# Performance work log

Measured on AMD Instinct MI355X. Metric: run time of the kernel, lower is better.

## Reference

```python
import jax, jax.numpy as jnp
import numpy as np

B, N, C, T, K = 32, 4096, 768, 1000, 20

def setup_inputs() -> dict:
    key = jax.random.key(0)
    k1, k2, k3, k4 = jax.random.split(key, 4)
    g_feat = jax.random.normal(k1, (B, 1, C), dtype=jnp.float32)
    inp = jax.random.normal(k2, (B, N, C), dtype=jnp.float32)
    tau = jax.random.uniform(k3, (1,), dtype=jnp.float32)
    text_embeddings = jax.random.normal(k4, (T, C), dtype=jnp.float32) * 0.01
    return {"g_feat": g_feat, "input": inp, "tau": tau, "text_embeddings": text_embeddings}


def reference(g_feat, input, tau, text_embeddings):
    feat = input  # [B, N, C]
    # 1x1 conv of global feature against text embeddings -> class logits [B, T]
    vg_logit = jnp.einsum('bc,tc->bt', g_feat[:, 0, :], text_embeddings)
    # top-20 candidate categories per image
    _, indices = jax.lax.top_k(vg_logit, K)              # [B, K]
    agg_text_features = text_embeddings[indices]          # [B, K, C] gather
    # per-pixel logits against the 20 gathered text embeddings
    seg_logit = jnp.exp(tau[0]) * jnp.einsum('bkc,bnc->bkn', agg_text_features, feat)  # [B, K, N]
    # hard (straight-through) softmax over candidate axis (dim=-2)
    y_soft = jax.nn.softmax(seg_logit, axis=-2)
    idx = jnp.argmax(seg_logit, axis=-2)                  # [B, N]
    y_hard = jnp.moveaxis(jax.nn.one_hot(idx, K, dtype=seg_logit.dtype), -1, -2)  # [B, K, N]
    attn = y_hard - jax.lax.stop_gradient(y_soft) + y_soft
    # normalize over pixel axis (assign_eps = 1.0)
    assign_attn = attn / (jnp.sum(attn, axis=-1, keepdims=True) + 1.0)
    # combine: [B, N, K] @ [B, K, C] -> [B, N, C]
    text_grids = jnp.einsum('bkn,bkc->bnc', assign_attn, agg_text_features)
    return text_grids
```

## Files before the change

kernel.cpp:

```cpp
#include <hip/hip_runtime.h>
#include <cfloat>

#define B_ 32
#define N_ 4096
#define C_ 768
#define T_ 1000
#define K_ 20

#define PXB 256
#define PHC 32
#define NPH (C_/PHC)
#define GAP_TH 1e-4f
#define MAXF 16384

typedef float f32x4 __attribute__((ext_vector_type(4)));
typedef int   i32x2 __attribute__((ext_vector_type(2)));
typedef short s16x8 __attribute__((ext_vector_type(8)));

__device__ __forceinline__ unsigned short bf_rne(float x) {
    unsigned u = __float_as_uint(x);
    return (unsigned short)((u + 0x7fffu + ((u >> 16) & 1u)) >> 16);
}

__global__ __launch_bounds__(256) void k1_logits(const float* __restrict__ g_feat,
                                                 const float* __restrict__ text,
                                                 double* __restrict__ logits,
                                                 int* __restrict__ cnt,
                                                 int* __restrict__ flagcnt) {
    int b = blockIdx.x;
    int wid = threadIdx.x >> 6, lane = threadIdx.x & 63;
    int t = blockIdx.y * 4 + wid;
    if (b == 0 && blockIdx.y == 0) {
        for (int i = threadIdx.x; i < B_ * K_; i += 256) cnt[i] = 0;
        if (threadIdx.x == 0) flagcnt[0] = 0;
    }
    const float* g = g_feat + b * C_;
    const float* e = text + t * C_;
    double s = 0.0;
    #pragma unroll
    for (int j = 0; j < 12; ++j) {
        int c = lane + 64 * j;
        s += (double)g[c] * (double)e[c];
    }
    #pragma unroll
    for (int m = 32; m; m >>= 1) s += __shfl_xor(s, m);
    if (lane == 0) logits[b * T_ + t] = s;
}

__global__ __launch_bounds__(256) void k1b_topk(const double* __restrict__ logits,
                                                const float* __restrict__ text,
                                                float* __restrict__ agg,
                                                unsigned short* __restrict__ Epk) {
    __shared__ unsigned short hiL[32 * C_];
    __shared__ unsigned short loL[32 * C_];
    __shared__ int ssel[K_];
    int b = blockIdx.x, tid = threadIdx.x, lane = tid & 63;
    if (tid < 64) {
        double v[16];
        #pragma unroll
        for (int j = 0; j < 16; ++j) {
            int t = lane + 64 * j;
            v[j] = (t < T_) ? logits[b * T_ + t] : -DBL_MAX;
        }
        for (int it = 0; it < K_; ++it) {
            double bv = -DBL_MAX; int bi = 0x7fffffff;
            #pragma unroll
            for (int j = 0; j < 16; ++j) {
                int t = lane + 64 * j;
                if (v[j] > bv) { bv = v[j]; bi = t; }
            }
            #pragma unroll
            for (int m = 32; m; m >>= 1) {
                double ov = __shfl_xor(bv, m); int oi = __shfl_xor(bi, m);
                if (ov > bv || (ov == bv && oi < bi)) { bv = ov; bi = oi; }
            }
            if (lane == 0) ssel[it] = bi;
            #pragma unroll
            for (int j = 0; j < 16; ++j) {
                int t = lane + 64 * j;
                if (t == bi) v[j] = -DBL_MAX;
            }
        }
    }
    __syncthreads();
    for (int i = tid; i < 32 * C_; i += 256) {
        int r = i / C_, c = i - r * C_;
        float v = (r < K_) ? text[ssel[r] * C_ + c] : 0.f;
        if (r < K_) agg[b * K_ * C_ + i] = v;
        unsigned u = __float_as_uint(v);
        float fh = __uint_as_float(u & 0xffff0000u);
        hiL[i] = (unsigned short)(u >> 16);
        loL[i] = bf_rne(v - fh);
    }
    __syncthreads();
    for (int i = tid; i < 24 * 256; i += 256) {
        int p = i >> 8, r = i & 255, f = r >> 6, ln = r & 63;
        int row = (f & 1) * 16 + (ln & 15);
        int col = p * 32 + (ln >> 4) * 8;
        const unsigned short* src = ((f < 2) ? hiL : loL) + row * C_ + col;
        *(s16x8*)(Epk + ((size_t)b * 6144 + i) * 8) = *(const s16x8*)src;
    }
}

__global__ __launch_bounds__(256, 4) void k2_argmax(const float* __restrict__ feat,
                                                    const unsigned short* __restrict__ Epk,
                                                    int* __restrict__ kidx,
                                                    int* __restrict__ cnt,
                                                    int* __restrict__ flagcnt,
                                                    int* __restrict__ flaglist) {
    __shared__ unsigned short hiT[PXB * PHC];
    __shared__ unsigned short loT[PXB * PHC];
    __shared__ int scnt[K_];
    int bx = blockIdx.x;
    int b = bx >> 4, tile = bx & 15;
    int n0 = tile * PXB;
    int tid = threadIdx.x, wid = tid >> 6, lane = tid & 63;
    if (tid < K_) scnt[tid] = 0;
    __syncthreads();

    const float* fb = feat + ((size_t)b * N_ + n0) * C_;
    const unsigned short* Eb = Epk + (size_t)b * 6144 * 8;
    int l3 = lane >> 3;
    int ch = lane & 7;
    int arow = lane & 15, acg = lane >> 4;

    f32x4 fr[8];
    auto LOADF = [&](int p) {
        #pragma unroll
        for (int i = 0; i < 8; ++i) {
            int row = wid * 64 + i * 8 + l3;
            fr[i] = *(const f32x4*)(fb + (size_t)row * C_ + p * PHC + ch * 4);
        }
    };
    auto CVTW = [&]() {
        int g = ch >> 1, h = ch & 1;
        #pragma unroll
        for (int i = 0; i < 8; ++i) {
            int row = wid * 64 + i * 8 + l3;
            unsigned u0 = __float_as_uint(fr[i].x), u1 = __float_as_uint(fr[i].y);
            unsigned u2 = __float_as_uint(fr[i].z), u3 = __float_as_uint(fr[i].w);
            unsigned ha = (u0 >> 16) | (u1 & 0xffff0000u);
            unsigned hb = (u2 >> 16) | (u3 & 0xffff0000u);
            unsigned la = (unsigned)bf_rne(fr[i].x - __uint_as_float(u0 & 0xffff0000u)) |
                          ((unsigned)bf_rne(fr[i].y - __uint_as_float(u1 & 0xffff0000u)) << 16);
            unsigned lb = (unsigned)bf_rne(fr[i].z - __uint_as_float(u2 & 0xffff0000u)) |
                          ((unsigned)bf_rne(fr[i].w - __uint_as_float(u3 & 0xffff0000u)) << 16);
            int a16 = row * PHC + ((g ^ (row & 3)) * 8) + h * 4;
            i32x2 hv = { (int)ha, (int)hb };
            i32x2 lv = { (int)la, (int)lb };
            *(i32x2*)&hiT[a16] = hv;
            *(i32x2*)&loT[a16] = lv;
        }
    };

    s16x8 Ach0, Ach1, Acl0, Acl1;
    auto LOADA = [&](int p) {
        const s16x8* ap = (const s16x8*)(Eb + (size_t)p * 256 * 8);
        Ach0 = ap[0 * 64 + lane];
        Ach1 = ap[1 * 64 + lane];
        Acl0 = ap[2 * 64 + lane];
        Acl1 = ap[3 * 64 + lane];
    };

    f32x4 acc0[4], acc1[4];
    #pragma unroll
    for (int i = 0; i < 4; ++i) { acc0[i] = (f32x4)0.f; acc1[i] = (f32x4)0.f; }

    LOADF(0);

    #pragma unroll 1
    for (int p = 0; p < NPH; ++p) {
        LOADA(p);
        asm volatile("s_waitcnt lgkmcnt(0)" ::: "memory");
        __builtin_amdgcn_sched_barrier(0);
        CVTW();
        if (p + 1 < NPH) LOADF(p + 1);
        asm volatile("s_waitcnt lgkmcnt(0)" ::: "memory");
        __builtin_amdgcn_sched_barrier(0);

        #pragma unroll
        for (int i = 0; i < 4; ++i) {
            int px = wid * 64 + i * 16 + arow;
            int a16 = px * PHC + (acg ^ (px & 3)) * 8;
            s16x8 Bh = *(const s16x8*)&hiT[a16];
            s16x8 Bl = *(const s16x8*)&loT[a16];
            acc0[i] = __builtin_amdgcn_mfma_f32_16x16x32_bf16(Ach0, Bh, acc0[i], 0, 0, 0);
            acc1[i] = __builtin_amdgcn_mfma_f32_16x16x32_bf16(Ach1, Bh, acc1[i], 0, 0, 0);
            acc0[i] = __builtin_amdgcn_mfma_f32_16x16x32_bf16(Ach0, Bl, acc0[i], 0, 0, 0);
            acc1[i] = __builtin_amdgcn_mfma_f32_16x16x32_bf16(Ach1, Bl, acc1[i], 0, 0, 0);
            acc0[i] = __builtin_amdgcn_mfma_f32_16x16x32_bf16(Acl0, Bh, acc0[i], 0, 0, 0);
            acc1[i] = __builtin_amdgcn_mfma_f32_16x16x32_bf16(Acl1, Bh, acc1[i], 0, 0, 0);
        }
    }

    #pragma unroll
    for (int i = 0; i < 4; ++i) {
        int kb = acg * 4;
        float m1 = acc0[i][0]; int i1 = kb; float m2 = -FLT_MAX;
        #pragma unroll
        for (int r = 1; r < 4; ++r) {
            float v = acc0[i][r];
            if (v > m1) { m2 = m1; m1 = v; i1 = kb + r; }
            else if (v > m2) m2 = v;
        }
        if (acg == 0) {
            #pragma unroll
            for (int r = 0; r < 4; ++r) {
                float v = acc1[i][r];
                if (v > m1) { m2 = m1; m1 = v; i1 = 16 + r; }
                else if (v > m2) m2 = v;
            }
        }
        #pragma unroll
        for (int s = 16; s < 64; s <<= 1) {
            float om1 = __shfl_xor(m1, s); int oi1 = __shfl_xor(i1, s);
            float om2 = __shfl_xor(m2, s);
            if (om1 > m1 || (om1 == m1 && oi1 < i1)) { m2 = fmaxf(m1, om2); m1 = om1; i1 = oi1; }
            else { m2 = fmaxf(m2, om1); }
        }
        if (lane < 16) {
            int n = n0 + wid * 64 + i * 16 + lane;
            kidx[b * N_ + n] = i1;
            atomicAdd(&scnt[i1], 1);
            if (m1 - m2 < GAP_TH) {
                int pos = atomicAdd(flagcnt, 1);
                if (pos < MAXF) flaglist[pos] = b * N_ + n;
            }
        }
    }
    __syncthreads();
    if (tid < K_) atomicAdd(&cnt[b * K_ + tid], scnt[tid]);
}

__global__ __launch_bounds__(256) void k25_refine(const float* __restrict__ feat,
                                                  const float* __restrict__ agg,
                                                  int* __restrict__ kidx,
                                                  int* __restrict__ cnt,
                                                  const int* __restrict__ flagcnt,
                                                  const int* __restrict__ flaglist) {
    int wid = threadIdx.x >> 6, lane = threadIdx.x & 63;
    int wg = blockIdx.x * 4 + wid;
    int nf = flagcnt[0]; if (nf > MAXF) nf = MAXF;
    for (int e = wg; e < nf; e += gridDim.x * 4) {
        int pix = flaglist[e];
        int b = pix >> 12;
        const float* fr = feat + (size_t)pix * C_;
        const float* ebase = agg + b * K_ * C_;
        double fd[12];
        #pragma unroll
        for (int j = 0; j < 12; ++j) fd[j] = (double)fr[lane + 64 * j];
        double best = -DBL_MAX; int bi = 0;
        for (int k = 0; k < K_; ++k) {
            const float* er = ebase + k * C_;
            double s = 0.0;
            #pragma unroll
            for (int j = 0; j < 12; ++j) s += fd[j] * (double)er[lane + 64 * j];
            #pragma unroll
            for (int m = 32; m; m >>= 1) s += __shfl_xor(s, m);
            if (s > best) { best = s; bi = k; }
        }
        if (lane == 0) {
            int old = kidx[pix];
            if (old != bi) {
                kidx[pix] = bi;
                atomicSub(&cnt[b * K_ + old], 1);
                atomicAdd(&cnt[b * K_ + bi], 1);
            }
        }
    }
}

__global__ __launch_bounds__(256) void k3s_scale(const float* __restrict__ agg,
                                                 const int* __restrict__ cnt,
                                                 float* __restrict__ sagg) {
    __shared__ float sc[K_];
    int b = blockIdx.x, tid = threadIdx.x;
    if (tid < K_) sc[tid] = 1.0f / ((float)cnt[b * K_ + tid] + 1.0f);
    __syncthreads();
    const f32x4* a4 = (const f32x4*)(agg + (size_t)b * K_ * C_);
    f32x4* s4 = (f32x4*)(sagg + (size_t)b * K_ * C_);
    #pragma unroll 1
    for (int i = tid; i < K_ * (C_ / 4); i += 256) {
        int k = i / (C_ / 4);
        s4[i] = a4[i] * sc[k];
    }
}

__global__ __launch_bounds__(256) void k4_out(const float* __restrict__ sagg,
                                              const int* __restrict__ kidx,
                                              float* __restrict__ out) {
    int wid = threadIdx.x >> 6, lane = threadIdx.x & 63;
    int wg = blockIdx.x * 4 + wid;
    int base = wg * 8;
    int b = base >> 12;
    int kk[8];
    #pragma unroll
    for (int i = 0; i < 8; ++i) kk[i] = kidx[base + i];
    const f32x4* sagg4 = (const f32x4*)sagg;
    f32x4* out4 = (f32x4*)out;

    f32x4 va0, va1, va2, vb0, vb1, vb2;
    {
        const f32x4* a4 = sagg4 + (size_t)(b * K_ + kk[0]) * (C_ / 4);
        va0 = a4[lane]; va1 = a4[lane + 64]; va2 = a4[lane + 128];
    }
    #pragma unroll
    for (int i = 0; i < 8; ++i) {
        if (i + 1 < 8) {
            const f32x4* a4 = sagg4 + (size_t)(b * K_ + kk[i + 1]) * (C_ / 4);
            vb0 = a4[lane]; vb1 = a4[lane + 64]; vb2 = a4[lane + 128];
        }
        f32x4* o4 = out4 + (size_t)(base + i) * (C_ / 4);
        o4[lane] = va0; o4[lane + 64] = va1; o4[lane + 128] = va2;
        va0 = vb0; va1 = vb1; va2 = vb2;
    }
}

extern "C" void kernel_launch(void* const* d_in, const int* in_sizes, int n_in,
                              void* d_out, int out_size, void* d_ws, size_t ws_size,
                              hipStream_t stream) {
    const float* g_feat = (const float*)d_in[0];
    const float* feat   = (const float*)d_in[1];
    const float* text   = (const float*)d_in[3];
    float* out = (float*)d_out;

    char* ws = (char*)d_ws;
    double* logits        = (double*)(ws + 0);
    float*  agg           = (float*) (ws + 262144);
    int*    cnt           = (int*)   (ws + 2230784);
    int*    flagc         = (int*)   (ws + 2233344);
    int*    flagl         = (int*)   (ws + 2233408);
    int*    kidx          = (int*)   (ws + 2301504);
    unsigned short* Epk   = (unsigned short*)(ws + 2825792);
    float*  sagg          = (float*) (ws + 5971520);

    k1_logits<<<dim3(32, 250), 256, 0, stream>>>(g_feat, text, logits, cnt, flagc);
    k1b_topk<<<32, 256, 0, stream>>>(logits, text, agg, Epk);
    k2_argmax<<<32 * 16, 256, 0, stream>>>(feat, Epk, kidx, cnt, flagc, flagl);
    k25_refine<<<1024, 256, 0, stream>>>(feat, agg, kidx, cnt, flagc, flagl);
    k3s_scale<<<32, 256, 0, stream>>>(agg, cnt, sagg);
    k4_out<<<4096, 256, 0, stream>>>(sagg, kidx, out);
}
```

Before: 272.3 us.

## Load feature tiles directly into MFMA B-fragments, dropping LDS staging in argmax kernel

The argmax kernel now has each wavefront own 16 pixels and load feature values straight from global memory in the MFMA B-operand layout, converting them to hi/lo bf16 in registers. This removes the LDS transpose buffers, the LDS writes and reads, and the waitcnt barriers. The grid grows to 2048 blocks and the occupancy hint rises to 6. The trade-off is that each lane's global loads are now only 32 bytes per row across 16 rows, which coalesces less well. The per-wave A-fragment reloads from Epk also happen four times as often relative to the pixels processed.

```diff
diff --git a/kernel.cpp b/kernel.cpp
--- a/kernel.cpp
+++ b/kernel.cpp
@@ -7,14 +7,13 @@
 #define T_ 1000
 #define K_ 20
 
-#define PXB 256
 #define PHC 32
 #define NPH (C_/PHC)
 #define GAP_TH 1e-4f
 #define MAXF 16384
 
 typedef float f32x4 __attribute__((ext_vector_type(4)));
-typedef int   i32x2 __attribute__((ext_vector_type(2)));
+typedef int   i32x4 __attribute__((ext_vector_type(4)));
 typedef short s16x8 __attribute__((ext_vector_type(8)));
 
 __device__ __forceinline__ unsigned short bf_rne(float x) {
@@ -102,130 +101,101 @@
     }
 }
 
-__global__ __launch_bounds__(256, 4) void k2_argmax(const float* __restrict__ feat,
+__global__ __launch_bounds__(256, 6) void k2_argmax(const float* __restrict__ feat,
                                                     const unsigned short* __restrict__ Epk,
                                                     int* __restrict__ kidx,
                                                     int* __restrict__ cnt,
                                                     int* __restrict__ flagcnt,
                                                     int* __restrict__ flaglist) {
-    __shared__ unsigned short hiT[PXB * PHC];
-    __shared__ unsigned short loT[PXB * PHC];
     __shared__ int scnt[K_];
-    int bx = blockIdx.x;
-    int b = bx >> 4, tile = bx & 15;
-    int n0 = tile * PXB;
     int tid = threadIdx.x, wid = tid >> 6, lane = tid & 63;
     if (tid < K_) scnt[tid] = 0;
     __syncthreads();
 
-    const float* fb = feat + ((size_t)b * N_ + n0) * C_;
+    int gw = blockIdx.x * 4 + wid;
+    int b  = gw >> 8;
+    int n0 = (gw & 255) * 16;
+    int prow = lane & 15;
+    int g    = lane >> 4;
+    const float* fp0 = feat + ((size_t)b * N_ + n0 + prow) * C_ + g * 8;
     const unsigned short* Eb = Epk + (size_t)b * 6144 * 8;
-    int l3 = lane >> 3;
-    int ch = lane & 7;
-    int arow = lane & 15, acg = lane >> 4;
-
-    f32x4 fr[8];
-    auto LOADF = [&](int p) {
-        #pragma unroll
-        for (int i = 0; i < 8; ++i) {
-            int row = wid * 64 + i * 8 + l3;
-            fr[i] = *(const f32x4*)(fb + (size_t)row * C_ + p * PHC + ch * 4);
-        }
-    };
-    auto CVTW = [&]() {
-        int g = ch >> 1, h = ch & 1;
-        #pragma unroll
-        for (int i = 0; i < 8; ++i) {
-            int row = wid * 64 + i * 8 + l3;
-            unsigned u0 = __float_as_uint(fr[i].x), u1 = __float_as_uint(fr[i].y);
-            unsigned u2 = __float_as_uint(fr[i].z), u3 = __float_as_uint(fr[i].w);
-            unsigned ha = (u0 >> 16) | (u1 & 0xffff0000u);
-            unsigned hb = (u2 >> 16) | (u3 & 0xffff0000u);
-            unsigned la = (unsigned)bf_rne(fr[i].x - __uint_as_float(u0 & 0xffff0000u)) |
-                          ((unsigned)bf_rne(fr[i].y - __uint_as_float(u1 & 0xffff0000u)) << 16);
-            unsigned lb = (unsigned)bf_rne(fr[i].z - __uint_as_float(u2 & 0xffff0000u)) |
-                          ((unsigned)bf_rne(fr[i].w - __uint_as_float(u3 & 0xffff0000u)) << 16);
-            int a16 = row * PHC + ((g ^ (row & 3)) * 8) + h * 4;
-            i32x2 hv = { (int)ha, (int)hb };
-            i32x2 lv = { (int)la, (int)lb };
-            *(i32x2*)&hiT[a16] = hv;
-            *(i32x2*)&loT[a16] = lv;
-        }
-    };
-
-    s16x8 Ach0, Ach1, Acl0, Acl1;
+
+    f32x4 fr0, fr1, nf0, nf1;
+    s16x8 Ah0, Ah1, Al0, Al1;
     auto LOADA = [&](int p) {
         const s16x8* ap = (const s16x8*)(Eb + (size_t)p * 256 * 8);
-        Ach0 = ap[0 * 64 + lane];
-        Ach1 = ap[1 * 64 + lane];
-        Acl0 = ap[2 * 64 + lane];
-        Acl1 = ap[3 * 64 + lane];
+        Ah0 = ap[lane]; Ah1 = ap[64 + lane];
+        Al0 = ap[128 + lane]; Al1 = ap[192 + lane];
     };
-
-    f32x4 acc0[4], acc1[4];
-    #pragma unroll
-    for (int i = 0; i < 4; ++i) { acc0[i] = (f32x4)0.f; acc1[i] = (f32x4)0.f; }
-
-    LOADF(0);
+    auto CVT = [&](f32x4 a, f32x4 c, s16x8& H, s16x8& L) {
+        float x[8] = { a.x, a.y, a.z, a.w, c.x, c.y, c.z, c.w };
+        unsigned hu[8], lu[8];
+        #pragma unroll
+        for (int j = 0; j < 8; ++j) {
+            unsigned u = __float_as_uint(x[j]);
+            hu[j] = u >> 16;
+            lu[j] = bf_rne(x[j] - __uint_as_float(u & 0xffff0000u));
+        }
+        i32x4 hv = { (int)(hu[0] | (hu[1] << 16)), (int)(hu[2] | (hu[3] << 16)),
+                     (int)(hu[4] | (hu[5] << 16)), (int)(hu[6] | (hu[7] << 16)) };
+        i32x4 lv = { (int)(lu[0] | (lu[1] << 16)), (int)(lu[2] | (lu[3] << 16)),
+                     (int)(lu[4] | (lu[5] << 16)), (int)(lu[6] | (lu[7] << 16)) };
+        H = __builtin_bit_cast(s16x8, hv);
+        L = __builtin_bit_cast(s16x8, lv);
+    };
+
+    f32x4 acc0 = (f32x4)0.f, acc1 = (f32x4)0.f;
+    fr0 = *(const f32x4*)(fp0);
+    fr1 = *(const f32x4*)(fp0 + 4);
 
     #pragma unroll 1
     for (int p = 0; p < NPH; ++p) {
+        if (p + 1 < NPH) {
+            nf0 = *(const f32x4*)(fp0 + (p + 1) * PHC);
+            nf1 = *(const f32x4*)(fp0 + (p + 1) * PHC + 4);
+        }
         LOADA(p);
-        asm volatile("s_waitcnt lgkmcnt(0)" ::: "memory");
-        __builtin_amdgcn_sched_barrier(0);
-        CVTW();
-        if (p + 1 < NPH) LOADF(p + 1);
-        asm volatile("s_waitcnt lgkmcnt(0)" ::: "memory");
-        __builtin_amdgcn_sched_barrier(0);
-
+        s16x8 Bh, Bl;
+        CVT(fr0, fr1, Bh, Bl);
+        acc0 = __builtin_amdgcn_mfma_f32_16x16x32_bf16(Ah0, Bh, acc0, 0, 0, 0);
+        acc1 = __builtin_amdgcn_mfma_f32_16x16x32_bf16(Ah1, Bh, acc1, 0, 0, 0);
+        acc0 = __builtin_amdgcn_mfma_f32_16x16x32_bf16(Ah0, Bl, acc0, 0, 0, 0);
+        acc1 = __builtin_amdgcn_mfma_f32_16x16x32_bf16(Ah1, Bl, acc1, 0, 0, 0);
+        acc0 = __builtin_amdgcn_mfma_f32_16x16x32_bf16(Al0, Bh, acc0, 0, 0, 0);
+        acc1 = __builtin_amdgcn_mfma_f32_16x16x32_bf16(Al1, Bh, acc1, 0, 0, 0);
+        fr0 = nf0; fr1 = nf1;
+    }
+
+    int kb = g * 4;
+    float m1 = acc0[0]; int i1 = kb; float m2 = -FLT_MAX;
+    #pragma unroll
+    for (int r = 1; r < 4; ++r) {
+        float v = acc0[r];
+        if (v > m1) { m2 = m1; m1 = v; i1 = kb + r; }
+        else if (v > m2) m2 = v;
+    }
+    if (g == 0) {
         #pragma unroll
-        for (int i = 0; i < 4; ++i) {
-            int px = wid * 64 + i * 16 + arow;
-            int a16 = px * PHC + (acg ^ (px & 3)) * 8;
-            s16x8 Bh = *(const s16x8*)&hiT[a16];
-            s16x8 Bl = *(const s16x8*)&loT[a16];
-            acc0[i] = __builtin_amdgcn_mfma_f32_16x16x32_bf16(Ach0, Bh, acc0[i], 0, 0, 0);
-            acc1[i] = __builtin_amdgcn_mfma_f32_16x16x32_bf16(Ach1, Bh, acc1[i], 0, 0, 0);
-            acc0[i] = __builtin_amdgcn_mfma_f32_16x16x32_bf16(Ach0, Bl, acc0[i], 0, 0, 0);
-            acc1[i] = __builtin_amdgcn_mfma_f32_16x16x32_bf16(Ach1, Bl, acc1[i], 0, 0, 0);
-            acc0[i] = __builtin_amdgcn_mfma_f32_16x16x32_bf16(Acl0, Bh, acc0[i], 0, 0, 0);
-            acc1[i] = __builtin_amdgcn_mfma_f32_16x16x32_bf16(Acl1, Bh, acc1[i], 0, 0, 0);
-        }
-    }
-
-    #pragma unroll
-    for (int i = 0; i < 4; ++i) {
-        int kb = acg * 4;
-        float m1 = acc0[i][0]; int i1 = kb; float m2 = -FLT_MAX;
-        #pragma unroll
-        for (int r = 1; r < 4; ++r) {
-            float v = acc0[i][r];
-            if (v > m1) { m2 = m1; m1 = v; i1 = kb + r; }
+        for (int r = 0; r < 4; ++r) {
+            float v = acc1[r];
+            if (v > m1) { m2 = m1; m1 = v; i1 = 16 + r; }
             else if (v > m2) m2 = v;
         }
-        if (acg == 0) {
-            #pragma unroll
-            for (int r = 0; r < 4; ++r) {
-                float v = acc1[i][r];
-                if (v > m1) { m2 = m1; m1 = v; i1 = 16 + r; }
-                else if (v > m2) m2 = v;
-            }
-        }
-        #pragma unroll
-        for (int s = 16; s < 64; s <<= 1) {
-            float om1 = __shfl_xor(m1, s); int oi1 = __shfl_xor(i1, s);
-            float om2 = __shfl_xor(m2, s);
-            if (om1 > m1 || (om1 == m1 && oi1 < i1)) { m2 = fmaxf(m1, om2); m1 = om1; i1 = oi1; }
-            else { m2 = fmaxf(m2, om1); }
-        }
-        if (lane < 16) {
-            int n = n0 + wid * 64 + i * 16 + lane;
-            kidx[b * N_ + n] = i1;
-            atomicAdd(&scnt[i1], 1);
-            if (m1 - m2 < GAP_TH) {
-                int pos = atomicAdd(flagcnt, 1);
-                if (pos < MAXF) flaglist[pos] = b * N_ + n;
-            }
+    }
+    #pragma unroll
+    for (int s = 16; s < 64; s <<= 1) {
+        float om1 = __shfl_xor(m1, s); int oi1 = __shfl_xor(i1, s);
+        float om2 = __shfl_xor(m2, s);
+        if (om1 > m1 || (om1 == m1 && oi1 < i1)) { m2 = fmaxf(m1, om2); m1 = om1; i1 = oi1; }
+        else { m2 = fmaxf(m2, om1); }
+    }
+    if (lane < 16) {
+        int n = n0 + lane;
+        kidx[b * N_ + n] = i1;
+        atomicAdd(&scnt[i1], 1);
+        if (m1 - m2 < GAP_TH) {
+            int pos = atomicAdd(flagcnt, 1);
+            if (pos < MAXF) flaglist[pos] = b * N_ + n;
         }
     }
     __syncthreads();
@@ -336,7 +306,7 @@
 
     k1_logits<<<dim3(32, 250), 256, 0, stream>>>(g_feat, text, logits, cnt, flagc);
     k1b_topk<<<32, 256, 0, stream>>>(logits, text, agg, Epk);
-    k2_argmax<<<32 * 16, 256, 0, stream>>>(feat, Epk, kidx, cnt, flagc, flagl);
+    k2_argmax<<<2048, 256, 0, stream>>>(feat, Epk, kidx, cnt, flagc, flagl);
     k25_refine<<<1024, 256, 0, stream>>>(feat, agg, kidx, cnt, flagc, flagl);
     k3s_scale<<<32, 256, 0, stream>>>(agg, cnt, sagg);
     k4_out<<<4096, 256, 0, stream>>>(sagg, kidx, out);
```

Result: slower. 283.1 us (+4.0%).
